# Kernel optimization log

Hardware: AMD Instinct MI355X
Metric: run time of the kernel (lower is better)

## Reference

```python
import jax, jax.numpy as jnp
import numpy as np

FH = FW = 3          # field_height, field_width
SF = 2               # scale_factor passed to set_transforms
NODES = 32           # out_channels
D_IN = 16            # in_channels (field depth)
HID = 32             # mlpnodes[0]; mlpnodes = [32, 1]


def maxpool_3x3_s2_p1(x):
    # Deterministic stand-in for FractionalMaxPool2d(kernel=3, output=(H//2, W//2)):
    return jax.lax.reduce_window(
        x, -jnp.inf, jax.lax.max,
        window_dimensions=(1, 1, 3, 3),
        window_strides=(1, 1, 2, 2),
        padding=((0, 0), (0, 0), (1, 1), (1, 1)))


def unfold_3x3(x):
    # torch.nn.Unfold(kernel=(3,3), padding=1): (N,D,H,W) -> (N, D, 9, H*W)
    N, D, H, W = x.shape
    xp = jnp.pad(x, ((0, 0), (0, 0), (1, 1), (1, 1)))
    patches = jnp.stack([xp[:, :, i:i + H, j:j + W]
                         for i in range(3) for j in range(3)], axis=2)
    return patches.reshape(N, D, 9, H * W)


def setup_inputs() -> dict:
    key = jax.random.key(0)
    k = jax.random.split(key, 6)
    N, H, W = 32, 96, 96
    x = jax.random.normal(k[0], (N, D_IN, H, W), dtype=jnp.float32)
    # S per node: xavier_uniform on shape (1, D, 3, 3): fan_in=D*9, fan_out=1*9
    bound_S = float(np.sqrt(6.0 / (D_IN * 9 + 9)))
    S = jax.random.uniform(k[1], (NODES, D_IN, FH, FW), jnp.float32, -bound_S, bound_S)
    # per-node MLP: Linear(D_IN -> HID) -> ReLU -> Linear(HID -> 1) -> ReLU
    b1w = 1.0 / np.sqrt(D_IN)
    W1 = jax.random.uniform(k[2], (NODES, D_IN, HID), jnp.float32, -b1w, b1w)
    b1 = jax.random.uniform(k[3], (NODES, HID), jnp.float32, -b1w, b1w)
    b2w = 1.0 / np.sqrt(HID)
    W2 = jax.random.uniform(k[4], (NODES, HID, 1), jnp.float32, -b2w, b2w)
    b2 = jax.random.uniform(k[5], (NODES, 1), jnp.float32, -b2w, b2w)
    return {"x": x, "S": S, "W1": W1, "b1": b1, "W2": W2, "b2": b2}


def reference(x, S, W1, b1, W2, b2):
    N, D, H, W = x.shape
    Hs, Ws = H // SF, W // SF
    U = unfold_3x3(maxpool_3x3_s2_p1(x))            # (N, D, 9, L), L = Hs*Ws
    Sf = S.reshape(S.shape[0], D, FH * FW)          # (O, D, 9)
    # StructFun: M[n,d,l] = sum_k S[d,k] * U[n,d,k,l], batched over nodes o
    M = jnp.einsum('odk,ndkl->nlod', Sf, U)         # (N, L, O, D)
    # StructBlock: reshape to (N,Hs,Ws,D) then per-node MLP over last dim
    h = jax.nn.relu(jnp.einsum('nlod,odh->nloh', M, W1) + b1)   # (N, L, O, HID)
    y = jax.nn.relu(jnp.einsum('nloh,ohe->nloe', h, W2) + b2)   # (N, L, O, 1)
    out = y[..., 0].reshape(N, Hs, Ws, -1)          # (N, Hs, Ws, O)
    return out.transpose(0, 3, 1, 2)                # (N, O, Hs, Ws)
```

## Files before the change

### kernel.cpp

```cpp
#include <hip/hip_runtime.h>
#include <math.h>

typedef __bf16 bf16;
typedef __bf16 bf16x8 __attribute__((ext_vector_type(8)));
typedef float  f32x16 __attribute__((ext_vector_type(16)));

#define D_INC 16
#define NODES 32
#define HID   32
#define HS    48
#define WSZ   48
#define NPX   (HS*WSZ)
#define H_IN  96
#define W_IN  96
#define N_B   32

__global__ __launch_bounds__(256) void wpre_kernel(
    const float* __restrict__ S, const float* __restrict__ W1,
    const float* __restrict__ b1, bf16* __restrict__ Wp)
{
    int idx = blockIdx.x * 256 + threadIdx.x;
    if (idx >= NODES * 10 * 2 * HID * 8) return;
    int j  = idx & 7;
    int h  = (idx >> 3) & 31;
    int qp = (idx >> 8) & 1;
    int os = idx >> 9;
    int s  = os % 10;
    int o  = os / 10;
    int k  = 16 * s + 8 * qp + j;
    float v = 0.f;
    if (k < 144) {
        int t = k >> 4;
        int d = k & 15;
        v = S[(o * D_INC + d) * 9 + t] * W1[(o * D_INC + d) * HID + h];
    } else if (k == 144) {
        v = b1[o * HID + h];
    }
    Wp[idx] = (bf16)v;
}

__global__ __launch_bounds__(256) void maxpool_kernel(
    const float* __restrict__ x, bf16* __restrict__ Pg)
{
    int idx = blockIdx.x * 256 + threadIdx.x;
    if (idx >= N_B * HS * WSZ) return;
    int c = idx % WSZ;
    int t = idx / WSZ;
    int r = t % HS;
    int n = t / HS;

    float m[D_INC];
    #pragma unroll
    for (int ch = 0; ch < D_INC; ++ch) m[ch] = -INFINITY;

    #pragma unroll
    for (int dr = 0; dr < 3; ++dr) {
        int xr = 2 * r - 1 + dr;
        if (xr < 0) continue;
        #pragma unroll
        for (int dc = 0; dc < 3; ++dc) {
            int xc = 2 * c - 1 + dc;
            bool ok = (xc >= 0);
            #pragma unroll
            for (int ch = 0; ch < D_INC; ++ch) {
                float v = ok ? x[((size_t)(n * D_INC + ch) * H_IN + xr) * W_IN + xc]
                             : -INFINITY;
                m[ch] = fmaxf(m[ch], v);
            }
        }
    }
    union { bf16 h[16]; uint4 q[2]; } u;
    #pragma unroll
    for (int ch = 0; ch < D_INC; ++ch) u.h[ch] = (bf16)m[ch];
    uint4* dst = (uint4*)(Pg + (size_t)idx * D_INC);
    dst[0] = u.q[0];
    dst[1] = u.q[1];
}

__global__ __launch_bounds__(256, 2) void gemm_kernel(
    const bf16* __restrict__ Pg, const bf16* __restrict__ Wp,
    const float* __restrict__ W2, const float* __restrict__ b2,
    float* __restrict__ out)
{
    __shared__ __align__(16) bf16  Pl[8 * 50 * D_INC];
    __shared__ __align__(16) float W2l[8 * HID];

    const int b    = blockIdx.x;
    const int n    = blockIdx.y;
    const int ob   = blockIdx.z * 8;
    const int tid  = threadIdx.x;
    const int lane = tid & 63;
    const int w    = tid >> 6;
    const int ln31 = lane & 31;
    const int qp   = lane >> 5;

    const int px0     = b * 256;
    const int r_start = px0 / 48;

    const uint4 z4 = make_uint4(0u, 0u, 0u, 0u);

    for (int u = tid; u < 768; u += 256) {
        int half = u & 1;
        int colu = (u >> 1) % 48;
        int row  = (u >> 1) / 48;
        int pr   = r_start - 1 + row;
        uint4 v  = z4;
        if (pr >= 0 && pr < HS)
            v = *(const uint4*)(Pg + ((size_t)(n * HS + pr) * WSZ + colu) * D_INC + half * 8);
        *(uint4*)(Pl + (row * 50 + colu + 1) * D_INC + half * 8) = v;
    }
    if (tid < 32) {
        int row  = tid >> 2;
        int side = (tid >> 1) & 1;
        int half = tid & 1;
        *(uint4*)(Pl + (row * 50 + side * 49) * D_INC + half * 8) = z4;
    }
    if (tid < 64)
        ((float4*)W2l)[tid] = ((const float4*)(W2 + ob * HID))[tid];
    __syncthreads();

    int base_ad[2];
    int pxg[2];
    #pragma unroll
    for (int t = 0; t < 2; ++t) {
        int px = px0 + w * 64 + t * 32 + ln31;
        int r  = px / 48;
        int c  = px - r * 48;
        int rl = r - r_start;
        base_ad[t] = ((rl * 50) + c) * 32 + qp * 16;
        pxg[t] = px;
    }

    bf16x8 Bf[2][10];
    #pragma unroll
    for (int t = 0; t < 2; ++t) {
        #pragma unroll
        for (int s = 0; s < 9; ++s) {
            const int di = s / 3, dj = s % 3;
            Bf[t][s] = *(const bf16x8*)((const char*)Pl + base_ad[t] + (di * 50 + dj) * 32);
        }
        bf16x8 bias = {};
        if (qp == 0) bias[0] = (bf16)1.0f;
        Bf[t][9] = bias;
    }

    for (int o8 = 0; o8 < 8; ++o8) {
        const int o = ob + o8;

        const bf16* wp = Wp + (size_t)(o * 10) * 512 + lane * 8;
        bf16x8 Af[10];
        #pragma unroll
        for (int s = 0; s < 10; ++s)
            Af[s] = *(const bf16x8*)(wp + s * 512);

        const float* w2b = W2l + o8 * HID + 4 * qp;
        float4 w2v0 = *(const float4*)(w2b);
        float4 w2v1 = *(const float4*)(w2b + 8);
        float4 w2v2 = *(const float4*)(w2b + 16);
        float4 w2v3 = *(const float4*)(w2b + 24);
        const float bb = b2[o];

        f32x16 acc0 = {};
        f32x16 acc1 = {};
        #pragma unroll
        for (int s = 0; s < 10; ++s) {
            acc0 = __builtin_amdgcn_mfma_f32_32x32x16_bf16(Af[s], Bf[0][s], acc0, 0, 0, 0);
            acc1 = __builtin_amdgcn_mfma_f32_32x32x16_bf16(Af[s], Bf[1][s], acc1, 0, 0, 0);
        }

        #pragma unroll
        for (int t = 0; t < 2; ++t) {
            const f32x16 a = t ? acc1 : acc0;
            float part;
            part  = fmaxf(a[0],  0.f) * w2v0.x;
            part  = fmaf(fmaxf(a[1],  0.f), w2v0.y, part);
            part  = fmaf(fmaxf(a[2],  0.f), w2v0.z, part);
            part  = fmaf(fmaxf(a[3],  0.f), w2v0.w, part);
            part  = fmaf(fmaxf(a[4],  0.f), w2v1.x, part);
            part  = fmaf(fmaxf(a[5],  0.f), w2v1.y, part);
            part  = fmaf(fmaxf(a[6],  0.f), w2v1.z, part);
            part  = fmaf(fmaxf(a[7],  0.f), w2v1.w, part);
            part  = fmaf(fmaxf(a[8],  0.f), w2v2.x, part);
            part  = fmaf(fmaxf(a[9],  0.f), w2v2.y, part);
            part  = fmaf(fmaxf(a[10], 0.f), w2v2.z, part);
            part  = fmaf(fmaxf(a[11], 0.f), w2v2.w, part);
            part  = fmaf(fmaxf(a[12], 0.f), w2v3.x, part);
            part  = fmaf(fmaxf(a[13], 0.f), w2v3.y, part);
            part  = fmaf(fmaxf(a[14], 0.f), w2v3.z, part);
            part  = fmaf(fmaxf(a[15], 0.f), w2v3.w, part);
            float tot = part + __shfl_xor(part, 32);
            tot = fmaxf(tot + bb, 0.f);
            if (qp == 0)
                out[(size_t)(n * NODES + o) * NPX + pxg[t]] = tot;
        }
    }
}

extern "C" void kernel_launch(void* const* d_in, const int* in_sizes, int n_in,
                              void* d_out, int out_size, void* d_ws, size_t ws_size,
                              hipStream_t stream)
{
    const float* x  = (const float*)d_in[0];
    const float* S  = (const float*)d_in[1];
    const float* W1 = (const float*)d_in[2];
    const float* b1 = (const float*)d_in[3];
    const float* W2 = (const float*)d_in[4];
    const float* b2 = (const float*)d_in[5];
    float* out = (float*)d_out;

    bf16* Pg = (bf16*)d_ws;
    bf16* Wp = (bf16*)((char*)d_ws + (size_t)N_B * NPX * D_INC * 2);

    wpre_kernel<<<640, 256, 0, stream>>>(S, W1, b1, Wp);
    maxpool_kernel<<<288, 256, 0, stream>>>(x, Pg);

    dim3 grid(9, N_B, 4);
    gemm_kernel<<<grid, 256, 0, stream>>>(Pg, Wp, W2, b2, out);
}
```

Baseline: 118.3 us.

## Merge preprocessing kernels, split maxpool channels across threads, double gemm grid

The weight-prep and maxpool kernels are merged into one launch, with block ranges dispatching to each role. Maxpool now assigns four threads per output pixel, each handling four channels, which raises thread-level parallelism from 288 to 1152 blocks and shortens each thread's serial load chain. The gemm grid doubles along the node axis (4 nodes per block instead of 8), giving more blocks for occupancy at the cost of reloading the pooled tile in twice as many blocks.

Result: faster. 107.9 us (-8.8%).

```diff
diff --git a/kernel.cpp b/kernel.cpp
--- a/kernel.cpp
+++ b/kernel.cpp
@@ -15,66 +15,63 @@
 #define W_IN  96
 #define N_B   32
 
-__global__ __launch_bounds__(256) void wpre_kernel(
+#define MP_BLOCKS   1152
+#define WPRE_BLOCKS 640
+
+__global__ __launch_bounds__(256) void pre_kernel(
+    const float* __restrict__ x, bf16* __restrict__ Pg,
     const float* __restrict__ S, const float* __restrict__ W1,
     const float* __restrict__ b1, bf16* __restrict__ Wp)
 {
-    int idx = blockIdx.x * 256 + threadIdx.x;
-    if (idx >= NODES * 10 * 2 * HID * 8) return;
-    int j  = idx & 7;
-    int h  = (idx >> 3) & 31;
-    int qp = (idx >> 8) & 1;
-    int os = idx >> 9;
-    int s  = os % 10;
-    int o  = os / 10;
-    int k  = 16 * s + 8 * qp + j;
-    float v = 0.f;
-    if (k < 144) {
-        int t = k >> 4;
-        int d = k & 15;
-        v = S[(o * D_INC + d) * 9 + t] * W1[(o * D_INC + d) * HID + h];
-    } else if (k == 144) {
-        v = b1[o * HID + h];
-    }
-    Wp[idx] = (bf16)v;
-}
-
-__global__ __launch_bounds__(256) void maxpool_kernel(
-    const float* __restrict__ x, bf16* __restrict__ Pg)
-{
-    int idx = blockIdx.x * 256 + threadIdx.x;
-    if (idx >= N_B * HS * WSZ) return;
-    int c = idx % WSZ;
-    int t = idx / WSZ;
-    int r = t % HS;
-    int n = t / HS;
-
-    float m[D_INC];
-    #pragma unroll
-    for (int ch = 0; ch < D_INC; ++ch) m[ch] = -INFINITY;
-
-    #pragma unroll
-    for (int dr = 0; dr < 3; ++dr) {
-        int xr = 2 * r - 1 + dr;
-        if (xr < 0) continue;
-        #pragma unroll
-        for (int dc = 0; dc < 3; ++dc) {
-            int xc = 2 * c - 1 + dc;
-            bool ok = (xc >= 0);
+    if (blockIdx.x < MP_BLOCKS) {
+        int idx = blockIdx.x * 256 + threadIdx.x;
+        int q = idx & 3;
+        int c = (idx >> 2) % WSZ;
+        int t = (idx >> 2) / WSZ;
+        int r = t % HS;
+        int n = t / HS;
+
+        const float* xb = x + ((size_t)(n * D_INC + q * 4)) * (H_IN * W_IN);
+
+        float m0 = -INFINITY, m1 = -INFINITY, m2 = -INFINITY, m3 = -INFINITY;
+        #pragma unroll
+        for (int dr = 0; dr < 3; ++dr) {
+            int xr = 2 * r - 1 + dr;
+            if (xr < 0) continue;
             #pragma unroll
-            for (int ch = 0; ch < D_INC; ++ch) {
-                float v = ok ? x[((size_t)(n * D_INC + ch) * H_IN + xr) * W_IN + xc]
-                             : -INFINITY;
-                m[ch] = fmaxf(m[ch], v);
+            for (int dc = 0; dc < 3; ++dc) {
+                int xc = 2 * c - 1 + dc;
+                if (xc < 0) continue;
+                const float* p = xb + xr * W_IN + xc;
+                m0 = fmaxf(m0, p[0 * H_IN * W_IN]);
+                m1 = fmaxf(m1, p[1 * H_IN * W_IN]);
+                m2 = fmaxf(m2, p[2 * H_IN * W_IN]);
+                m3 = fmaxf(m3, p[3 * H_IN * W_IN]);
             }
         }
-    }
-    union { bf16 h[16]; uint4 q[2]; } u;
-    #pragma unroll
-    for (int ch = 0; ch < D_INC; ++ch) u.h[ch] = (bf16)m[ch];
-    uint4* dst = (uint4*)(Pg + (size_t)idx * D_INC);
-    dst[0] = u.q[0];
-    dst[1] = u.q[1];
+        union { bf16 h[4]; uint2 u; } v;
+        v.h[0] = (bf16)m0; v.h[1] = (bf16)m1; v.h[2] = (bf16)m2; v.h[3] = (bf16)m3;
+        *(uint2*)(Pg + (size_t)idx * 4) = v.u;
+    } else {
+        int idx = (blockIdx.x - MP_BLOCKS) * 256 + threadIdx.x;
+        if (idx >= NODES * 10 * 2 * HID * 8) return;
+        int j  = idx & 7;
+        int h  = (idx >> 3) & 31;
+        int qp = (idx >> 8) & 1;
+        int os = idx >> 9;
+        int s  = os % 10;
+        int o  = os / 10;
+        int k  = 16 * s + 8 * qp + j;
+        float v = 0.f;
+        if (k < 144) {
+            int t = k >> 4;
+            int d = k & 15;
+            v = S[(o * D_INC + d) * 9 + t] * W1[(o * D_INC + d) * HID + h];
+        } else if (k == 144) {
+            v = b1[o * HID + h];
+        }
+        Wp[idx] = (bf16)v;
+    }
 }
 
 __global__ __launch_bounds__(256, 2) void gemm_kernel(
@@ -83,11 +80,11 @@
     float* __restrict__ out)
 {
     __shared__ __align__(16) bf16  Pl[8 * 50 * D_INC];
-    __shared__ __align__(16) float W2l[8 * HID];
+    __shared__ __align__(16) float W2l[4 * HID];
 
     const int b    = blockIdx.x;
     const int n    = blockIdx.y;
-    const int ob   = blockIdx.z * 8;
+    const int ob   = blockIdx.z * 4;
     const int tid  = threadIdx.x;
     const int lane = tid & 63;
     const int w    = tid >> 6;
@@ -115,7 +112,7 @@
         int half = tid & 1;
         *(uint4*)(Pl + (row * 50 + side * 49) * D_INC + half * 8) = z4;
     }
-    if (tid < 64)
+    if (tid < 32)
         ((float4*)W2l)[tid] = ((const float4*)(W2 + ob * HID))[tid];
     __syncthreads();
 
@@ -144,8 +141,8 @@
         Bf[t][9] = bias;
     }
 
-    for (int o8 = 0; o8 < 8; ++o8) {
-        const int o = ob + o8;
+    for (int o4 = 0; o4 < 4; ++o4) {
+        const int o = ob + o4;
 
         const bf16* wp = Wp + (size_t)(o * 10) * 512 + lane * 8;
         bf16x8 Af[10];
@@ -153,7 +150,7 @@
         for (int s = 0; s < 10; ++s)
             Af[s] = *(const bf16x8*)(wp + s * 512);
 
-        const float* w2b = W2l + o8 * HID + 4 * qp;
+        const float* w2b = W2l + o4 * HID + 4 * qp;
         float4 w2v0 = *(const float4*)(w2b);
         float4 w2v1 = *(const float4*)(w2b + 8);
         float4 w2v2 = *(const float4*)(w2b + 16);
@@ -211,9 +208,8 @@
     bf16* Pg = (bf16*)d_ws;
     bf16* Wp = (bf16*)((char*)d_ws + (size_t)N_B * NPX * D_INC * 2);
 
-    wpre_kernel<<<640, 256, 0, stream>>>(S, W1, b1, Wp);
-    maxpool_kernel<<<288, 256, 0, stream>>>(x, Pg);
-
-    dim3 grid(9, N_B, 4);
+    pre_kernel<<<MP_BLOCKS + WPRE_BLOCKS, 256, 0, stream>>>(x, Pg, S, W1, b1, Wp);
+
+    dim3 grid(9, N_B, 8);
     gemm_kernel<<<grid, 256, 0, stream>>>(Pg, Wp, W2, b2, out);
 }
```
